# Optimization experiments

Measured on AMD Instinct MI355X. Metric: run time of the kernel, lower is better.

## Reference

```python
import jax, jax.numpy as jnp
import numpy as np
from jax import lax

EPS = 1e-6
DT_RANK = 24  # ceil(384/16), Mamba convention
D_STATE = 16


def _ln(x, g, b, eps=EPS):
    m = jnp.mean(x, axis=-1, keepdims=True)
    v = jnp.mean((x - m) ** 2, axis=-1, keepdims=True)
    return (x - m) * lax.rsqrt(v + eps) * g + b


def setup_inputs() -> dict:
    key = jax.random.key(0)
    ks = jax.random.split(key, 10)
    B, Dd, Hh, Ww, C = 2, 8, 16, 16, 384
    di, ds, r = 384, D_STATE, DT_RANK  # d_inner = expand * d_model = 384
    s = 0.02
    f = lambda k, shape: (jax.random.normal(k, shape, jnp.float32) * s)
    return {
        "x": jax.random.normal(ks[0], (B, Dd, Hh, Ww, C), jnp.float32),
        "g1": jnp.ones((C,), jnp.float32), "b1": jnp.zeros((C,), jnp.float32),
        "W_in": f(ks[1], (C, 2 * di)), "b_in": jnp.zeros((2 * di,), jnp.float32),
        "conv_w": f(ks[2], (di, 1, 3, 3, 3)), "conv_b": jnp.zeros((di,), jnp.float32),
        "W_x": f(ks[3], (di, r + 2 * ds)),
        "W_dt": f(ks[4], (r, di)), "b_dt": jnp.zeros((di,), jnp.float32),
        "A_log": jnp.tile(jnp.log(jnp.arange(1, ds + 1, dtype=jnp.float32)), (di, 1)),
        "D_skip": jnp.ones((di,), jnp.float32),
        "on_g": jnp.ones((di,), jnp.float32), "on_b": jnp.zeros((di,), jnp.float32),
        "W_out": f(ks[5], (di, C)), "b_out": jnp.zeros((C,), jnp.float32),
        "g2": jnp.ones((C,), jnp.float32), "b2": jnp.zeros((C,), jnp.float32),
        "W1": f(ks[6], (C, C)), "b1m": jnp.zeros((C,), jnp.float32),
        "W2": f(ks[7], (C, C)), "b2m": jnp.zeros((C,), jnp.float32),
    }


def _ss3d(h, W_in, b_in, conv_w, conv_b, W_x, W_dt, b_dt, A_log, D_skip, on_g, on_b, W_out, b_out):
    # h: [B, D, H, W, C] -> Mamba-style selective scan over flattened DHW (orientation 0)
    B, Dd, Hh, Ww, C = h.shape
    di = W_in.shape[1] // 2
    ds = D_STATE
    L = Dd * Hh * Ww
    seq = h.reshape(B, L, C)
    xz = seq @ W_in + b_in                      # [B, L, 2*di]
    xin, z = jnp.split(xz, 2, axis=-1)
    # depthwise 3D conv + SiLU on the x branch
    xc = xin.reshape(B, Dd, Hh, Ww, di).transpose(0, 4, 1, 2, 3)  # [B, di, D, H, W]
    xc = lax.conv_general_dilated(xc, conv_w, (1, 1, 1), 'SAME',
                                  feature_group_count=di,
                                  dimension_numbers=('NCDHW', 'OIDHW', 'NCDHW'))
    xc = xc + conv_b[None, :, None, None, None]
    xin = jax.nn.silu(xc).transpose(0, 2, 3, 4, 1).reshape(B, L, di)
    # input-dependent dt, B, C
    dbc = xin @ W_x                              # [B, L, r + 2*ds]
    dt, Bm, Cm = jnp.split(dbc, [DT_RANK, DT_RANK + ds], axis=-1)
    dt = jax.nn.softplus(dt @ W_dt + b_dt)       # [B, L, di]
    A = -jnp.exp(A_log)                          # [di, ds]
    dA = jnp.exp(dt[..., None] * A)              # [B, L, di, ds]
    dBx = dt[..., None] * Bm[:, :, None, :] * xin[..., None]  # [B, L, di, ds]

    def step(carry, inp):
        da, dbx, c = inp                         # [B,di,ds], [B,di,ds], [B,ds]
        carry = da * carry + dbx
        y = jnp.einsum('bds,bs->bd', carry, c)
        return carry, y

    xs = (dA.transpose(1, 0, 2, 3), dBx.transpose(1, 0, 2, 3), Cm.transpose(1, 0, 2))
    h0 = jnp.zeros((B, di, ds), dA.dtype)
    _, ys = lax.scan(step, h0, xs)               # ys: [L, B, di]
    y = ys.transpose(1, 0, 2) + xin * D_skip
    y = _ln(y, on_g, on_b) * jax.nn.silu(z)
    out = y @ W_out + b_out
    return out.reshape(B, Dd, Hh, Ww, C)


def reference(x, g1, b1, W_in, b_in, conv_w, conv_b, W_x, W_dt, b_dt, A_log, D_skip,
              on_g, on_b, W_out, b_out, g2, b2, W1, b1m, W2, b2m):
    # x + SS3D(LN(x)); then x + MLP(LN(x)).  drop_path/dropout = 0 (eval)
    a = _ss3d(_ln(x, g1, b1), W_in, b_in, conv_w, conv_b, W_x, W_dt, b_dt,
              A_log, D_skip, on_g, on_b, W_out, b_out)
    x1 = x + a
    h2 = _ln(x1, g2, b2)
    mlp = jax.nn.gelu(h2 @ W1 + b1m) @ W2 + b2m
    return x1 + mlp
```

## Files before the change

### kernel.cpp

```cpp
#include <hip/hip_runtime.h>
#include <hip/hip_bf16.h>

using bf16 = __hip_bfloat16;
#define DEV __device__ __forceinline__

typedef __attribute__((ext_vector_type(8))) short short8;
typedef __attribute__((ext_vector_type(8))) unsigned short ushort8;
typedef __attribute__((ext_vector_type(4))) float f32x4;

constexpr int Bb = 2, DD = 8, HH = 16, WW = 16;
constexpr int C = 384, DI = 384, DS = 16, RR = 24;
constexpr int L = DD * HH * WW;
constexpr int M = Bb * L;

DEV bf16 f2b(float v) { return __float2bfloat16(v); }
DEV unsigned short f2bu(float v) {
    bf16 t = __float2bfloat16(v);
    unsigned short u; __builtin_memcpy(&u, &t, 2); return u;
}
DEV float braw(unsigned short u) {
    unsigned int x = ((unsigned int)u) << 16;
    float f; __builtin_memcpy(&f, &x, 4); return f;
}
DEV bool isbf(const unsigned short* g1p) { return g1p[0] == 0x3F80; }

typedef const __attribute__((address_space(1))) unsigned int* gaddr_t;
typedef __attribute__((address_space(3))) unsigned int* laddr_t;
DEV void gload_lds16(const void* g, void* l) {
    __builtin_amdgcn_global_load_lds((gaddr_t)g, (laddr_t)l, 16, 0, 0);
}

DEV float wred64(float v) {
    #pragma unroll
    for (int off = 32; off > 0; off >>= 1) v += __shfl_xor(v, off, 64);
    return v;
}
DEV float siluf(float x) { return x / (1.0f + __expf(-x)); }
DEV float softplusf(float x) { return (x > 15.0f) ? x : log1pf(__expf(x)); }
DEV float gelu_tanh(float x) {
    const float k0 = 0.7978845608028654f;
    float u = k0 * (x + 0.044715f * x * x * x);
    float e = __expf(2.0f * u);
    float t = 1.0f - 2.0f / (e + 1.0f);
    return 0.5f * x * (1.0f + t);
}

struct PrepTab {
    const void* tsrc[4];
    unsigned short* tdst[4];
    int tK[4], tN[4];
    const void* csrc[17];
    float* cdst[17];
    int coff[18];
};
__global__ __launch_bounds__(256) void prep_k(PrepTab t,
                                              const void* __restrict__ xraw,
                                              const void* __restrict__ g1raw,
                                              const void* __restrict__ b1raw,
                                              bf16* __restrict__ hb,
                                              const unsigned short* __restrict__ g1p,
                                              int ctotal) {
    bool fl = isbf(g1p);
    int z = blockIdx.z;
    if (z < 4) {
        if (blockIdx.x >= 288) return;
        __shared__ unsigned short tt[32][33];
        int N = t.tN[z], K = t.tK[z];
        int n0 = (blockIdx.x % 24) * 32, k0 = (blockIdx.x / 24) * 32;
        if (n0 >= N || k0 >= K) return;
        const void* src = t.tsrc[z];
        unsigned short* dst = t.tdst[z];
        int tx = threadIdx.x & 31, ty = threadIdx.x >> 5;
        #pragma unroll
        for (int i = 0; i < 4; i++) {
            int k = k0 + ty + i * 8;
            unsigned short u;
            if (fl) u = ((const unsigned short*)src)[(size_t)k * N + n0 + tx];
            else    u = f2bu(((const float*)src)[(size_t)k * N + n0 + tx]);
            tt[ty + i * 8][tx] = u;
        }
        __syncthreads();
        #pragma unroll
        for (int i = 0; i < 4; i++) {
            int n = n0 + ty + i * 8;
            dst[(size_t)n * K + k0 + tx] = tt[tx][ty + i * 8];
        }
    } else if (z == 4) {
        int i = blockIdx.x * 256 + threadIdx.x;
        if (i >= ctotal) return;
        int seg = 0;
        #pragma unroll
        for (int k = 1; k < 18; k++) seg += (i >= t.coff[k]) ? 1 : 0;
        int j = i - t.coff[seg];
        const void* s = t.csrc[seg];
        float v = fl ? braw(((const unsigned short*)s)[j]) : ((const float*)s)[j];
        t.cdst[seg][j] = v;
    } else {
        int wave = blockIdx.x * 4 + (threadIdx.x >> 6);
        int lane = threadIdx.x & 63;
        size_t base = (size_t)wave * C;
        float v[6];
        #pragma unroll
        for (int j = 0; j < 6; j++) {
            size_t idx = base + lane + 64 * j;
            if (fl) v[j] = braw(((const unsigned short*)xraw)[idx]);
            else    v[j] = ((const float*)xraw)[idx];
        }
        float s = 0.f;
        #pragma unroll
        for (int j = 0; j < 6; j++) s += v[j];
        s = wred64(s);
        float mean = s * (1.0f / C);
        float q = 0.f;
        #pragma unroll
        for (int j = 0; j < 6; j++) { float d = v[j] - mean; q += d * d; }
        q = wred64(q);
        float rstd = rsqrtf(q * (1.0f / C) + 1e-6f);
        #pragma unroll
        for (int j = 0; j < 6; j++) {
            int c = lane + 64 * j;
            float gv, bv;
            if (fl) { gv = braw(((const unsigned short*)g1raw)[c]);
                      bv = braw(((const unsigned short*)b1raw)[c]); }
            else    { gv = ((const float*)g1raw)[c];
                      bv = ((const float*)b1raw)[c]; }
            hb[base + c] = f2b((v[j] - mean) * rstd * gv + bv);
        }
    }
}

__global__ __launch_bounds__(256) void ln_k(const float* __restrict__ x,
                                            const float* __restrict__ g,
                                            const float* __restrict__ b,
                                            bf16* __restrict__ out) {
    int wave = blockIdx.x * 4 + (threadIdx.x >> 6);
    int lane = threadIdx.x & 63;
    size_t base = (size_t)wave * C;
    float v[6];
    #pragma unroll
    for (int j = 0; j < 6; j++) v[j] = x[base + lane + 64 * j];
    float s = 0.f;
    #pragma unroll
    for (int j = 0; j < 6; j++) s += v[j];
    s = wred64(s);
    float mean = s * (1.0f / C);
    float q = 0.f;
    #pragma unroll
    for (int j = 0; j < 6; j++) { float d = v[j] - mean; q += d * d; }
    q = wred64(q);
    float rstd = rsqrtf(q * (1.0f / C) + 1e-6f);
    #pragma unroll
    for (int j = 0; j < 6; j++) {
        int c = lane + 64 * j;
        out[base + c] = f2b((v[j] - mean) * rstd * g[c] + b[c]);
    }
}

enum { EPI_XZT = 0, EPI_OUT = 1, EPI_GELU = 2, EPI_FINAL = 3 };

template <int N, int TN, int EPI>
__global__ __launch_bounds__(256) void gemm_mfma(const bf16* __restrict__ A,
                                                 const unsigned short* __restrict__ Bt,
                                                 const float* __restrict__ bias,
                                                 float* __restrict__ o0,
                                                 float* __restrict__ o1,
                                                 const float* __restrict__ auxf,
                                                 const void* __restrict__ auxraw,
                                                 void* __restrict__ obf,
                                                 const unsigned short* __restrict__ g1p) {
    __shared__ unsigned short Asb[128 * 32];
    __shared__ unsigned short Bsb[TN * 32];
    constexpr int MT = (TN == 128) ? 4 : 2;
    int tid = threadIdx.x;
    int m0 = blockIdx.x * 128, n0 = blockIdx.y * TN;
    int wid = tid >> 6, lane = tid & 63;
    int wm = (TN == 128) ? (wid >> 1) * 64 : wid * 32;
    int wn = (TN == 128) ? (wid & 1) * 64 : 0;
    int quad = lane >> 4, l15 = lane & 15;
    f32x4 acc[MT][4] = {};
    int srow = tid >> 2, sseg = (tid & 3) * 8;
    const unsigned short* Au = (const unsigned short*)A;
    for (int k0 = 0; k0 < 384; k0 += 32) {
        __syncthreads();
        gload_lds16(Au + (size_t)(m0 + srow) * 384 + k0 + sseg,
                    &Asb[srow * 32 + sseg]);
        gload_lds16(Au + (size_t)(m0 + 64 + srow) * 384 + k0 + sseg,
                    &Asb[(64 + srow) * 32 + sseg]);
        gload_lds16(Bt + (size_t)(n0 + srow) * 384 + k0 + sseg,
                    &Bsb[srow * 32 + sseg]);
        if constexpr (TN == 128)
            gload_lds16(Bt + (size_t)(n0 + 64 + srow) * 384 + k0 + sseg,
                        &Bsb[(64 + srow) * 32 + sseg]);
        __syncthreads();
        short8 af[MT], bfr[4];
        #pragma unroll
        for (int mt = 0; mt < MT; mt++)
            af[mt] = *(const short8*)&Asb[(wm + mt * 16 + l15) * 32 + quad * 8];
        #pragma unroll
        for (int nt = 0; nt < 4; nt++)
            bfr[nt] = *(const short8*)&Bsb[(wn + nt * 16 + l15) * 32 + quad * 8];
        #pragma unroll
        for (int mt = 0; mt < MT; mt++)
            #pragma unroll
            for (int nt = 0; nt < 4; nt++)
                acc[mt][nt] = __builtin_amdgcn_mfma_f32_16x16x32_bf16(
                    af[mt], bfr[nt], acc[mt][nt], 0, 0, 0);
    }
    bool fl = (EPI == EPI_FINAL || EPI == EPI_OUT) ? isbf(g1p) : false;
    #pragma unroll
    for (int mt = 0; mt < MT; mt++) {
        #pragma unroll
        for (int nt = 0; nt < 4; nt++) {
            int n = n0 + wn + nt * 16 + l15;
            int mb = m0 + wm + mt * 16 + quad * 4;
            float bi = bias[n];
            if constexpr (EPI == EPI_XZT) {
                f32x4 v = acc[mt][nt];
                v[0] += bi; v[1] += bi; v[2] += bi; v[3] += bi;
                float* dst = (n < 384) ? (o0 + (size_t)n * M + mb)
                                       : (o1 + (size_t)(n - 384) * M + mb);
                *(f32x4*)dst = v;
            } else {
                #pragma unroll
                for (int r = 0; r < 4; r++) {
                    int m = mb + r;
                    float v = acc[mt][nt][r] + bi;
                    if constexpr (EPI == EPI_OUT) {
                        float av;
                        if (fl) av = braw(((const unsigned short*)auxraw)[(size_t)m * 384 + n]);
                        else    av = ((const float*)auxraw)[(size_t)m * 384 + n];
                        o0[(size_t)m * 384 + n] = v + av;
                    } else if constexpr (EPI == EPI_GELU) {
                        ((bf16*)obf)[(size_t)m * 384 + n] = f2b(gelu_tanh(v));
                    } else {
                        float rr = v + auxf[(size_t)m * 384 + n];
                        if (fl) ((bf16*)obf)[(size_t)m * 384 + n] = f2b(rr);
                        else    ((float*)obf)[(size_t)m * 384 + n] = rr;
                    }
                }
            }
        }
    }
}

__global__ __launch_bounds__(256) void convT_k(const float* __restrict__ xT,
                                               const float* __restrict__ cw,
                                               const float* __restrict__ cb,
                                               float* __restrict__ xinT) {
    int c = blockIdx.y;
    int m0 = (blockIdx.x * 256 + threadIdx.x) * 4;
    int l = m0 & (L - 1);
    int d = l >> 8, h = (l >> 4) & 15, w0 = l & 15;
    const float* xc = xT + (size_t)c * M;
    const float* wc = cw + c * 27;
    float bias = cb[c];
    float acc[4] = {bias, bias, bias, bias};
    #pragma unroll
    for (int kd = -1; kd <= 1; kd++) {
        int dd = d + kd; if ((unsigned)dd >= 8u) continue;
        #pragma unroll
        for (int kh = -1; kh <= 1; kh++) {
            int hh = h + kh; if ((unsigned)hh >= 16u) continue;
            int mm = m0 + kd * 256 + kh * 16;
            float vv[6];
            vv[0] = (w0 == 0) ? 0.f : xc[mm - 1];
            float4 v14 = *(const float4*)(xc + mm);
            vv[1] = v14.x; vv[2] = v14.y; vv[3] = v14.z; vv[4] = v14.w;
            vv[5] = (w0 == 12) ? 0.f : xc[mm + 4];
            const float* wk = wc + (kd + 1) * 9 + (kh + 1) * 3;
            float wa = wk[0], wb = wk[1], wcc = wk[2];
            #pragma unroll
            for (int j = 0; j < 4; j++)
                acc[j] = fmaf(vv[j], wa, fmaf(vv[j + 1], wb, fmaf(vv[j + 2], wcc, acc[j])));
        }
    }
    float4 o = make_float4(siluf(acc[0]), siluf(acc[1]), siluf(acc[2]), siluf(acc[3]));
    *(float4*)(xinT + (size_t)c * M + m0) = o;
}

__global__ __launch_bounds__(256) void dbc2_k(const float* __restrict__ xinT,
                                              const float* __restrict__ Wx,
                                              float* __restrict__ part) {
    __shared__ float As[16][64];
    __shared__ float Ws[16 * 56];
    int tid = threadIdx.x;
    int m0 = blockIdx.x * 64;
    int kc = blockIdx.y;
    int tm = tid & 63, grp = tid >> 6;
    int kk = tid >> 4, mc = (tid & 15) * 4;
    float acc[14] = {};
    for (int k0 = kc * 64; k0 < kc * 64 + 64; k0 += 16) {
        float4 av = *(const float4*)(xinT + (size_t)(k0 + kk) * M + m0 + mc);
        __syncthreads();
        *(float4*)&As[kk][mc] = av;
        for (int idx = tid; idx < 16 * 56; idx += 256)
            Ws[idx] = Wx[k0 * 56 + idx];
        __syncthreads();
        #pragma unroll
        for (int k = 0; k < 16; k++) {
            float a = As[k][tm];
            #pragma unroll
            for (int jj = 0; jj < 14; jj++)
                acc[jj] = fmaf(a, Ws[k * 56 + grp * 14 + jj], acc[jj]);
        }
    }
    int m = m0 + tm;
    #pragma unroll
    for (int jj = 0; jj < 14; jj++) {
        int col = grp * 14 + jj;
        part[((size_t)kc * 56 + col) * M + m] = acc[jj];
    }
}

__global__ __launch_bounds__(256) void dbcfin_k(const float* __restrict__ part,
                                                const float* __restrict__ Wdt,
                                                const float* __restrict__ bdt,
                                                float* __restrict__ dtT,
                                                unsigned short* __restrict__ Brow,
                                                unsigned short* __restrict__ Crow) {
    __shared__ float dtr[24][64];
    int tid = threadIdx.x;
    int m0 = blockIdx.x * 64;
    int ng = blockIdx.y;
    for (int i = tid; i < 24 * 64; i += 256) {
        int col = i >> 6, mm = i & 63;
        float s = 0.f;
        #pragma unroll
        for (int kc = 0; kc < 6; kc++)
            s += part[((size_t)kc * 56 + col) * M + m0 + mm];
        dtr[col][mm] = s;
    }
    if (ng == 0) {
        for (int i = tid; i < 32 * 64; i += 256) {
            int col = 24 + (i >> 6), mm = i & 63;
            float s = 0.f;
            #pragma unroll
            for (int kc = 0; kc < 6; kc++)
                s += part[((size_t)kc * 56 + col) * M + m0 + mm];
            int m = m0 + mm;
            if (col < 40) Brow[(size_t)m * 16 + col - 24] = f2bu(s);
            else          Crow[(size_t)m * 16 + col - 40] = f2bu(s);
        }
    }
    __syncthreads();
    int mm = tid & 63, nq = tid >> 6;
    #pragma unroll 4
    for (int nj = 0; nj < 16; nj++) {
        int n = ng * 64 + nq * 16 + nj;
        float acc = bdt[n];
        #pragma unroll
        for (int j = 0; j < 24; j++)
            acc = fmaf(dtr[j][mm], Wdt[j * 384 + n], acc);
        dtT[(size_t)n * M + m0 + mm] = softplusf(acc);
    }
}

__global__ __launch_bounds__(128) void scan4_k(const float* __restrict__ dtT,
                                               const float* __restrict__ xinT,
                                               const unsigned short* __restrict__ Brow,
                                               const unsigned short* __restrict__ Crow,
                                               const float* __restrict__ alog,
                                               const float* __restrict__ dsk,
                                               float* __restrict__ yT) {
    __shared__ float dt_s[2112], x_s[2112];
    __shared__ float ypart[2 * 2112];
    int bi = blockIdx.x;
    int b = bi / DI, d = bi % DI;
    int wave = threadIdx.x >> 6, lane = threadIdx.x & 63;
    int s0 = wave * 8;
    float Aneg[8];
    #pragma unroll
    for (int ss = 0; ss < 8; ss++) Aneg[ss] = -__expf(alog[d * DS + s0 + ss]);
    const float* dtp = dtT + (size_t)d * M + b * L;
    const float* xp  = xinT + (size_t)d * M + b * L;
    #pragma unroll
    for (int i = 0; i < 4; i++) {
        int t4 = (threadIdx.x + i * 128) * 4;
        float4 dv = *(const float4*)(dtp + t4);
        float4 xv = *(const float4*)(xp + t4);
        int base = t4 + (t4 >> 5);
        dt_s[base + 0] = dv.x; dt_s[base + 1] = dv.y;
        dt_s[base + 2] = dv.z; dt_s[base + 3] = dv.w;
        x_s[base + 0] = xv.x; x_s[base + 1] = xv.y;
        x_s[base + 2] = xv.z; x_s[base + 3] = xv.w;
    }
    __syncthreads();
    const unsigned short* Bp = Brow + ((size_t)b * L) * 16 + s0;
    const unsigned short* Cp = Crow + ((size_t)b * L) * 16 + s0;
    int tbase = lane * 32;
    int pbase = lane * 33;
    float Ap[8], Bg[8];
    #pragma unroll
    for (int ss = 0; ss < 8; ss++) { Ap[ss] = 1.f; Bg[ss] = 0.f; }
    #pragma unroll 4
    for (int j = 0; j < 32; j++) {
        float dtv = dt_s[pbase + j];
        float dxv = dtv * x_s[pbase + j];
        ushort8 bu = *(const ushort8*)(Bp + (size_t)(tbase + j) * 16);
        #pragma unroll
        for (int ss = 0; ss < 8; ss++) {
            float dA = __expf(dtv * Aneg[ss]);
            Bg[ss] = fmaf(dA, Bg[ss], dxv * braw(bu[ss]));
            Ap[ss] *= dA;
        }
    }
    float carry[8];
    #pragma unroll
    for (int ss = 0; ss < 8; ss++) {
        float a = Ap[ss], bb = Bg[ss];
        #pragma unroll
        for (int off = 1; off < 64; off <<= 1) {
            float ap = __shfl_up(a, off, 64);
            float bp = __shfl_up(bb, off, 64);
            if (lane >= off) { bb = fmaf(a, bp, bb); a *= ap; }
        }
        float c = __shfl_up(bb, 1, 64);
        carry[ss] = (lane == 0) ? 0.f : c;
    }
    float* ypw = ypart + wave * 2112;
    float h[8];
    #pragma unroll
    for (int ss = 0; ss < 8; ss++) h[ss] = carry[ss];
    #pragma unroll 4
    for (int j = 0; j < 32; j++) {
        float dtv = dt_s[pbase + j];
        float dxv = dtv * x_s[pbase + j];
        size_t toff = (size_t)(tbase + j) * 16;
        ushort8 bu = *(const ushort8*)(Bp + toff);
        ushort8 cu = *(const ushort8*)(Cp + toff);
        float acc = 0.f;
        #pragma unroll
        for (int ss = 0; ss < 8; ss++) {
            float dA = __expf(dtv * Aneg[ss]);
            h[ss] = fmaf(dA, h[ss], dxv * braw(bu[ss]));
            acc = fmaf(h[ss], braw(cu[ss]), acc);
        }
        ypw[pbase + j] = acc;
    }
    __syncthreads();
    float Dv = dsk[d];
    float* yp = yT + (size_t)d * M + b * L;
    #pragma unroll
    for (int i = 0; i < 16; i++) {
        int t = threadIdx.x + 128 * i;
        int ti = t + (t >> 5);
        yp[t] = fmaf(x_s[ti], Dv, ypart[ti] + ypart[2112 + ti]);
    }
}

__global__ __launch_bounds__(256) void lnmulT_k(const float* __restrict__ yT,
                                                const float* __restrict__ zT,
                                                const float* __restrict__ g,
                                                const float* __restrict__ b,
                                                unsigned short* __restrict__ yact) {
    __shared__ float rs1[8][32], rs2[8][32];
    __shared__ float meanb[32], rstdb[32];
    __shared__ unsigned short tile[32][392];
    int moff = threadIdx.x & 31;
    int dsub = threadIdx.x >> 5;
    int m0 = blockIdx.x * 32;
    size_t mg = m0 + moff;
    float s1 = 0.f, s2 = 0.f;
    #pragma unroll 8
    for (int j = 0; j < 48; j++) {
        int d = dsub + 8 * j;
        float v = yT[(size_t)d * M + mg];
        s1 += v; s2 += v * v;
    }
    rs1[dsub][moff] = s1;
    rs2[dsub][moff] = s2;
    __syncthreads();
    if (threadIdx.x < 32) {
        float a1 = 0.f, a2 = 0.f;
        #pragma unroll
        for (int ss = 0; ss < 8; ss++) { a1 += rs1[ss][threadIdx.x]; a2 += rs2[ss][threadIdx.x]; }
        float mean = a1 * (1.0f / DI);
        float var = a2 * (1.0f / DI) - mean * mean;
        meanb[threadIdx.x] = mean;
        rstdb[threadIdx.x] = rsqrtf(var + 1e-6f);
    }
    __syncthreads();
    float mean = meanb[moff], rstd = rstdb[moff];
    #pragma unroll 8
    for (int j = 0; j < 48; j++) {
        int d = dsub + 8 * j;
        float v = yT[(size_t)d * M + mg];
        float ln = (v - mean) * rstd * g[d] + b[d];
        float zv = zT[(size_t)d * M + mg];
        tile[moff][d] = f2bu(ln * siluf(zv));
    }
    __syncthreads();
    #pragma unroll
    for (int i = 0; i < 6; i++) {
        int chunk = threadIdx.x + 256 * i;
        int row = chunk / 48, cc = chunk % 48;
        *(uint4*)(yact + ((size_t)(m0 + row)) * 384 + cc * 8) =
            *(const uint4*)&tile[row][cc * 8];
    }
}

extern "C" void kernel_launch(void* const* d_in, const int* in_sizes, int n_in,
                              void* d_out, int out_size, void* d_ws, size_t ws_size,
                              hipStream_t stream) {
    float* ws = (float*)d_ws;
    constexpr size_t S = (size_t)M * 384;
    bf16*  hb   = (bf16*)ws;
    float* xT   = ws + S / 2;
    float* zT   = xT + S;
    float* xinT = zT + S;
    float* dtT  = xinT + S;
    float* x1   = dtT + S;
    unsigned short* Brow = (unsigned short*)(x1 + S);
    unsigned short* Crow = Brow + (size_t)M * 16;
    float* part = (float*)(Crow + (size_t)M * 16);
    float* smalls = part + (size_t)6 * 56 * M;

    float* g1f  = smalls;        float* b1f  = g1f + 384;
    float* binf = b1f + 384;     float* cwf  = binf + 768;
    float* cbf  = cwf + 10368;   float* wxf  = cbf + 384;
    float* wdtf = wxf + 21504;   float* bdtf = wdtf + 9216;
    float* alogf= bdtf + 384;    float* dskf = alogf + 6144;
    float* ongf = dskf + 384;    float* onbf = ongf + 384;
    float* boutf= onbf + 384;    float* g2f  = boutf + 384;
    float* b2f_ = g2f + 384;     float* b1mf = b2f_ + 384;
    float* b2mf = b1mf + 384;
    unsigned short* WinT  = (unsigned short*)(b2mf + 384);
    unsigned short* WoutT = WinT + 294912;
    unsigned short* W1T   = WoutT + 147456;
    unsigned short* W2T   = W1T + 147456;

    float* yT = xT;
    bf16* h2b = hb;
    unsigned short* yactb = (unsigned short*)dtT;
    unsigned short* m1b = (unsigned short*)zT;
    const unsigned short* g1p = (const unsigned short*)d_in[1];

    PrepTab tab;
    {
        tab.tsrc[0] = d_in[3];  tab.tdst[0] = WinT;  tab.tK[0] = 384; tab.tN[0] = 768;
        tab.tsrc[1] = d_in[14]; tab.tdst[1] = WoutT; tab.tK[1] = 384; tab.tN[1] = 384;
        tab.tsrc[2] = d_in[18]; tab.tdst[2] = W1T;   tab.tK[2] = 384; tab.tN[2] = 384;
        tab.tsrc[3] = d_in[20]; tab.tdst[3] = W2T;   tab.tK[3] = 384; tab.tN[3] = 384;
        int idxs[17] = {1, 2, 4, 5, 6, 7, 8, 9, 10, 11, 12, 13, 15, 16, 17, 19, 21};
        float* dsts[17] = {g1f, b1f, binf, cwf, cbf, wxf, wdtf, bdtf, alogf, dskf,
                           ongf, onbf, boutf, g2f, b2f_, b1mf, b2mf};
        int ns[17] = {384, 384, 768, 10368, 384, 21504, 9216, 384, 6144, 384,
                      384, 384, 384, 384, 384, 384, 384};
        int off = 0;
        for (int k = 0; k < 17; k++) {
            tab.csrc[k] = d_in[idxs[k]];
            tab.cdst[k] = dsts[k];
            tab.coff[k] = off;
            off += ns[k];
        }
        tab.coff[17] = off;
        prep_k<<<dim3(1024, 1, 6), 256, 0, stream>>>(
            tab, d_in[0], d_in[1], d_in[2], hb, g1p, off);
    }

    gemm_mfma<768, 128, EPI_XZT><<<dim3(M / 128, 6), 256, 0, stream>>>(
        hb, WinT, binf, xT, zT, nullptr, nullptr, nullptr, g1p);
    convT_k<<<dim3(M / 1024, DI), 256, 0, stream>>>(xT, cwf, cbf, xinT);
    dbc2_k<<<dim3(M / 64, 6), 256, 0, stream>>>(xinT, wxf, part);
    dbcfin_k<<<dim3(M / 64, 6), 256, 0, stream>>>(part, wdtf, bdtf, dtT, Brow, Crow);
    scan4_k<<<Bb * DI, 128, 0, stream>>>(dtT, xinT, Brow, Crow, alogf, dskf, yT);
    lnmulT_k<<<M / 32, 256, 0, stream>>>(yT, zT, ongf, onbf, yactb);
    gemm_mfma<384, 64, EPI_OUT><<<dim3(M / 128, 6), 256, 0, stream>>>(
        (const bf16*)yactb, WoutT, boutf, x1, nullptr, nullptr, d_in[0], nullptr, g1p);
    ln_k<<<M / 4, 256, 0, stream>>>(x1, g2f, b2f_, h2b);
    gemm_mfma<384, 64, EPI_GELU><<<dim3(M / 128, 6), 256, 0, stream>>>(
        h2b, W1T, b1mf, nullptr, nullptr, nullptr, nullptr, m1b, g1p);
    gemm_mfma<384, 64, EPI_FINAL><<<dim3(M / 128, 6), 256, 0, stream>>>(
        (const bf16*)m1b, W2T, b2mf, nullptr, nullptr, x1, nullptr, d_out, g1p);
}
```

Baseline: 237.0 us.

## Fold W_x·W_dt into combined weight and compute dt/B/C with one MFMA GEMM

Precomputes a combined bf16 weight matrix (W_x[:, :24] @ W_dt for dt, plus the B/C columns of W_x, padded to 448 rows) in the prep kernel. A single MFMA-based GEMM kernel then produces dt (with bias and softplus), B and C directly from xin. This replaces the split-K fp32 FMA kernel and its partial-sum reduction kernel, removing a launch and the large partial buffer traffic. It trades fp32 accumulation through the low-rank bottleneck for bf16 inputs over a full-rank 384x384 product, which changes rounding and does more FLOPs.

```diff
diff --git a/kernel.cpp b/kernel.cpp
--- a/kernel.cpp
+++ b/kernel.cpp
@@ -57,7 +57,10 @@
                                               const void* __restrict__ xraw,
                                               const void* __restrict__ g1raw,
                                               const void* __restrict__ b1raw,
+                                              const void* __restrict__ wxraw,
+                                              const void* __restrict__ wdtraw,
                                               bf16* __restrict__ hb,
+                                              unsigned short* __restrict__ Wall,
                                               const unsigned short* __restrict__ g1p,
                                               int ctotal) {
     bool fl = isbf(g1p);
@@ -95,7 +98,7 @@
         const void* s = t.csrc[seg];
         float v = fl ? braw(((const unsigned short*)s)[j]) : ((const float*)s)[j];
         t.cdst[seg][j] = v;
-    } else {
+    } else if (z == 5) {
         int wave = blockIdx.x * 4 + (threadIdx.x >> 6);
         int lane = threadIdx.x & 63;
         size_t base = (size_t)wave * C;
@@ -126,6 +129,30 @@
                       bv = ((const float*)b1raw)[c]; }
             hb[base + c] = f2b((v[j] - mean) * rstd * gv + bv);
         }
+    } else {
+        int i = blockIdx.x * 256 + threadIdx.x;
+        if (i >= 448 * 384) return;
+        int n = i / 384, k = i % 384;
+        float v;
+        if (n < 384) {
+            float acc = 0.f;
+            #pragma unroll
+            for (int j = 0; j < 24; j++) {
+                float wx = fl ? braw(((const unsigned short*)wxraw)[k * 56 + j])
+                              : ((const float*)wxraw)[k * 56 + j];
+                float wd = fl ? braw(((const unsigned short*)wdtraw)[j * 384 + n])
+                              : ((const float*)wdtraw)[j * 384 + n];
+                acc = fmaf(wx, wd, acc);
+            }
+            v = acc;
+        } else if (n < 416) {
+            int s = n - 384 + 24;
+            v = fl ? braw(((const unsigned short*)wxraw)[k * 56 + s])
+                   : ((const float*)wxraw)[k * 56 + s];
+        } else {
+            v = 0.f;
+        }
+        Wall[(size_t)n * 384 + k] = f2bu(v);
     }
 }
 
@@ -243,6 +270,79 @@
     }
 }
 
+__global__ __launch_bounds__(256) void dtbc_k(const float* __restrict__ xinT,
+                                              const unsigned short* __restrict__ Wall,
+                                              const float* __restrict__ bdt,
+                                              float* __restrict__ dtT,
+                                              unsigned short* __restrict__ Brow,
+                                              unsigned short* __restrict__ Crow) {
+    __shared__ float Asf[32][132];
+    __shared__ unsigned short Bsb[64 * 32];
+    int tid = threadIdx.x;
+    int m0 = blockIdx.x * 128, n0 = blockIdx.y * 64;
+    int wid = tid >> 6, lane = tid & 63;
+    int wm = wid * 32;
+    int quad = lane >> 4, l15 = lane & 15;
+    f32x4 acc[2][4] = {};
+    int srow = tid >> 2, sseg = (tid & 3) * 8;
+    for (int k0 = 0; k0 < 384; k0 += 32) {
+        __syncthreads();
+        #pragma unroll
+        for (int i = 0; i < 4; i++) {
+            int idx = tid + 256 * i;
+            int row = idx >> 5, c4 = (idx & 31) * 4;
+            float4 v = *(const float4*)(xinT + (size_t)(k0 + row) * M + m0 + c4);
+            *(float4*)&Asf[row][c4] = v;
+        }
+        gload_lds16(Wall + (size_t)(n0 + srow) * 384 + k0 + sseg,
+                    &Bsb[srow * 32 + sseg]);
+        __syncthreads();
+        short8 af[2], bfr[4];
+        #pragma unroll
+        for (int mt = 0; mt < 2; mt++) {
+            int ml = wm + mt * 16 + l15;
+            unsigned short u[8];
+            #pragma unroll
+            for (int j = 0; j < 8; j++) u[j] = f2bu(Asf[quad * 8 + j][ml]);
+            __builtin_memcpy(&af[mt], u, 16);
+        }
+        #pragma unroll
+        for (int nt = 0; nt < 4; nt++)
+            bfr[nt] = *(const short8*)&Bsb[(nt * 16 + l15) * 32 + quad * 8];
+        #pragma unroll
+        for (int mt = 0; mt < 2; mt++)
+            #pragma unroll
+            for (int nt = 0; nt < 4; nt++)
+                acc[mt][nt] = __builtin_amdgcn_mfma_f32_16x16x32_bf16(
+                    af[mt], bfr[nt], acc[mt][nt], 0, 0, 0);
+    }
+    #pragma unroll
+    for (int mt = 0; mt < 2; mt++) {
+        #pragma unroll
+        for (int nt = 0; nt < 4; nt++) {
+            int n = n0 + nt * 16 + l15;
+            int mb = m0 + wm + mt * 16 + quad * 4;
+            if (n < 384) {
+                float bi = bdt[n];
+                f32x4 v;
+                #pragma unroll
+                for (int r = 0; r < 4; r++) v[r] = softplusf(acc[mt][nt][r] + bi);
+                *(f32x4*)(dtT + (size_t)n * M + mb) = v;
+            } else if (n < 400) {
+                int s = n - 384;
+                #pragma unroll
+                for (int r = 0; r < 4; r++)
+                    Brow[(size_t)(mb + r) * 16 + s] = f2bu(acc[mt][nt][r]);
+            } else if (n < 416) {
+                int s = n - 400;
+                #pragma unroll
+                for (int r = 0; r < 4; r++)
+                    Crow[(size_t)(mb + r) * 16 + s] = f2bu(acc[mt][nt][r]);
+            }
+        }
+    }
+}
+
 __global__ __launch_bounds__(256) void convT_k(const float* __restrict__ xT,
                                                const float* __restrict__ cw,
                                                const float* __restrict__ cb,
@@ -276,83 +376,6 @@
     }
     float4 o = make_float4(siluf(acc[0]), siluf(acc[1]), siluf(acc[2]), siluf(acc[3]));
     *(float4*)(xinT + (size_t)c * M + m0) = o;
-}
-
-__global__ __launch_bounds__(256) void dbc2_k(const float* __restrict__ xinT,
-                                              const float* __restrict__ Wx,
-                                              float* __restrict__ part) {
-    __shared__ float As[16][64];
-    __shared__ float Ws[16 * 56];
-    int tid = threadIdx.x;
-    int m0 = blockIdx.x * 64;
-    int kc = blockIdx.y;
-    int tm = tid & 63, grp = tid >> 6;
-    int kk = tid >> 4, mc = (tid & 15) * 4;
-    float acc[14] = {};
-    for (int k0 = kc * 64; k0 < kc * 64 + 64; k0 += 16) {
-        float4 av = *(const float4*)(xinT + (size_t)(k0 + kk) * M + m0 + mc);
-        __syncthreads();
-        *(float4*)&As[kk][mc] = av;
-        for (int idx = tid; idx < 16 * 56; idx += 256)
-            Ws[idx] = Wx[k0 * 56 + idx];
-        __syncthreads();
-        #pragma unroll
-        for (int k = 0; k < 16; k++) {
-            float a = As[k][tm];
-            #pragma unroll
-            for (int jj = 0; jj < 14; jj++)
-                acc[jj] = fmaf(a, Ws[k * 56 + grp * 14 + jj], acc[jj]);
-        }
-    }
-    int m = m0 + tm;
-    #pragma unroll
-    for (int jj = 0; jj < 14; jj++) {
-        int col = grp * 14 + jj;
-        part[((size_t)kc * 56 + col) * M + m] = acc[jj];
-    }
-}
-
-__global__ __launch_bounds__(256) void dbcfin_k(const float* __restrict__ part,
-                                                const float* __restrict__ Wdt,
-                                                const float* __restrict__ bdt,
-                                                float* __restrict__ dtT,
-                                                unsigned short* __restrict__ Brow,
-                                                unsigned short* __restrict__ Crow) {
-    __shared__ float dtr[24][64];
-    int tid = threadIdx.x;
-    int m0 = blockIdx.x * 64;
-    int ng = blockIdx.y;
-    for (int i = tid; i < 24 * 64; i += 256) {
-        int col = i >> 6, mm = i & 63;
-        float s = 0.f;
-        #pragma unroll
-        for (int kc = 0; kc < 6; kc++)
-            s += part[((size_t)kc * 56 + col) * M + m0 + mm];
-        dtr[col][mm] = s;
-    }
-    if (ng == 0) {
-        for (int i = tid; i < 32 * 64; i += 256) {
-            int col = 24 + (i >> 6), mm = i & 63;
-            float s = 0.f;
-            #pragma unroll
-            for (int kc = 0; kc < 6; kc++)
-                s += part[((size_t)kc * 56 + col) * M + m0 + mm];
-            int m = m0 + mm;
-            if (col < 40) Brow[(size_t)m * 16 + col - 24] = f2bu(s);
-            else          Crow[(size_t)m * 16 + col - 40] = f2bu(s);
-        }
-    }
-    __syncthreads();
-    int mm = tid & 63, nq = tid >> 6;
-    #pragma unroll 4
-    for (int nj = 0; nj < 16; nj++) {
-        int n = ng * 64 + nq * 16 + nj;
-        float acc = bdt[n];
-        #pragma unroll
-        for (int j = 0; j < 24; j++)
-            acc = fmaf(dtr[j][mm], Wdt[j * 384 + n], acc);
-        dtT[(size_t)n * M + m0 + mm] = softplusf(acc);
-    }
 }
 
 __global__ __launch_bounds__(128) void scan4_k(const float* __restrict__ dtT,
@@ -512,13 +535,11 @@
     float* x1   = dtT + S;
     unsigned short* Brow = (unsigned short*)(x1 + S);
     unsigned short* Crow = Brow + (size_t)M * 16;
-    float* part = (float*)(Crow + (size_t)M * 16);
-    float* smalls = part + (size_t)6 * 56 * M;
-
-    float* g1f  = smalls;        float* b1f  = g1f + 384;
-    float* binf = b1f + 384;     float* cwf  = binf + 768;
-    float* cbf  = cwf + 10368;   float* wxf  = cbf + 384;
-    float* wdtf = wxf + 21504;   float* bdtf = wdtf + 9216;
+    unsigned short* WallT = Crow + (size_t)M * 16;
+    float* smalls = (float*)(WallT + (size_t)448 * 384);
+
+    float* binf = smalls;        float* cwf  = binf + 768;
+    float* cbf  = cwf + 10368;   float* bdtf = cbf + 384;
     float* alogf= bdtf + 384;    float* dskf = alogf + 6144;
     float* ongf = dskf + 384;    float* onbf = ongf + 384;
     float* boutf= onbf + 384;    float* g2f  = boutf + 384;
@@ -541,28 +562,28 @@
         tab.tsrc[1] = d_in[14]; tab.tdst[1] = WoutT; tab.tK[1] = 384; tab.tN[1] = 384;
         tab.tsrc[2] = d_in[18]; tab.tdst[2] = W1T;   tab.tK[2] = 384; tab.tN[2] = 384;
         tab.tsrc[3] = d_in[20]; tab.tdst[3] = W2T;   tab.tK[3] = 384; tab.tN[3] = 384;
-        int idxs[17] = {1, 2, 4, 5, 6, 7, 8, 9, 10, 11, 12, 13, 15, 16, 17, 19, 21};
-        float* dsts[17] = {g1f, b1f, binf, cwf, cbf, wxf, wdtf, bdtf, alogf, dskf,
-                           ongf, onbf, boutf, g2f, b2f_, b1mf, b2mf};
-        int ns[17] = {384, 384, 768, 10368, 384, 21504, 9216, 384, 6144, 384,
-                      384, 384, 384, 384, 384, 384, 384};
+        int idxs[13] = {4, 5, 6, 9, 10, 11, 12, 13, 15, 16, 17, 19, 21};
+        float* dsts[13] = {binf, cwf, cbf, bdtf, alogf, dskf, ongf, onbf,
+                           boutf, g2f, b2f_, b1mf, b2mf};
+        int ns[13] = {768, 10368, 384, 384, 6144, 384, 384, 384,
+                      384, 384, 384, 384, 384};
         int off = 0;
-        for (int k = 0; k < 17; k++) {
+        for (int k = 0; k < 13; k++) {
             tab.csrc[k] = d_in[idxs[k]];
             tab.cdst[k] = dsts[k];
             tab.coff[k] = off;
             off += ns[k];
         }
+        for (int k = 13; k < 17; k++) { tab.csrc[k] = d_in[21]; tab.cdst[k] = b2mf; tab.coff[k] = off; }
         tab.coff[17] = off;
-        prep_k<<<dim3(1024, 1, 6), 256, 0, stream>>>(
-            tab, d_in[0], d_in[1], d_in[2], hb, g1p, off);
+        prep_k<<<dim3(1024, 1, 7), 256, 0, stream>>>(
+            tab, d_in[0], d_in[1], d_in[2], d_in[7], d_in[8], hb, WallT, g1p, off);
     }
 
     gemm_mfma<768, 128, EPI_XZT><<<dim3(M / 128, 6), 256, 0, stream>>>(
         hb, WinT, binf, xT, zT, nullptr, nullptr, nullptr, g1p);
     convT_k<<<dim3(M / 1024, DI), 256, 0, stream>>>(xT, cwf, cbf, xinT);
-    dbc2_k<<<dim3(M / 64, 6), 256, 0, stream>>>(xinT, wxf, part);
-    dbcfin_k<<<dim3(M / 64, 6), 256, 0, stream>>>(part, wdtf, bdtf, dtT, Brow, Crow);
+    dtbc_k<<<dim3(M / 128, 7), 256, 0, stream>>>(xinT, WallT, bdtf, dtT, Brow, Crow);
     scan4_k<<<Bb * DI, 128, 0, stream>>>(dtT, xinT, Brow, Crow, alogf, dskf, yT);
     lnmulT_k<<<M / 32, 256, 0, stream>>>(yT, zT, ongf, onbf, yactb);
     gemm_mfma<384, 64, EPI_OUT><<<dim3(M / 128, 6), 256, 0, stream>>>(
```

After: 248.3 us. 4.8% more time.
